# Kernel optimization log

Measured on AMD Instinct MI355X. Metric: run time of the kernel, lower is better.

The kernel has to match this reference:

```python
import jax, jax.numpy as jnp
import numpy as np

TOP_K = 2  # k experts per token


def setup_inputs() -> dict:
    key = jax.random.key(0)
    ks = jax.random.split(key, 6)
    B, L, D, E, F = 2, 2048, 1024, 8, 4096
    x = jax.random.normal(ks[0], (B, L, D), dtype=jnp.float32)
    Wg = jax.random.normal(ks[1], (D, E), dtype=jnp.float32) * (D ** -0.5)
    W1 = jax.random.normal(ks[2], (E, D, F), dtype=jnp.float32) * (D ** -0.5)
    b1 = jnp.zeros((E, F), dtype=jnp.float32)
    W2 = jax.random.normal(ks[3], (E, F, D), dtype=jnp.float32) * (F ** -0.5)
    b2 = jnp.zeros((E, D), dtype=jnp.float32)
    return {"x": x, "Wg": Wg, "W1": W1, "b1": b1, "W2": W2, "b2": b2}


def reference(x, Wg, W1, b1, W2, b2):
    b, l, d = x.shape
    E = Wg.shape[1]
    xt = x.reshape(b * l, d)                      # (N, D)
    N = xt.shape[0]
    # Router: sigmoid gate, top-k (gate weights are NOT renormalized in the source)
    S = jax.nn.sigmoid(xt @ Wg)                   # (N, E)
    G, I = jax.lax.top_k(S, TOP_K)                # (N, k) each
    # Dense equivalent of per-expert gather-MLP-scatter: run every expert
    # on every token, then combine with the sparse top-k routing weights.
    h = jax.nn.gelu(jnp.einsum('nd,edf->enf', xt, W1) + b1[:, None, :])  # (E, N, F)
    y = jnp.einsum('enf,efd->end', h, W2) + b2[:, None, :]               # (E, N, D)
    # combine[n, e] = sum of gate values for slots routed to expert e
    combine = jnp.zeros((N, E), dtype=x.dtype).at[jnp.arange(N)[:, None], I].add(G)
    out = jnp.einsum('ne,end->nd', combine, y)    # (N, D)
    return out.reshape(b, l, d)
```

## Files before the change

kernel.cpp:

```cpp
#include <hip/hip_runtime.h>
#include <math.h>

typedef __bf16 bf16_t;
typedef __attribute__((ext_vector_type(8))) __bf16 bf16x8;
typedef __attribute__((ext_vector_type(4))) __bf16 bf16x4;
typedef __attribute__((ext_vector_type(4))) float f32x4;

#define NTOK 4096
#define DDIM 1024
#define FDIM 4096
#define NEXP 8
#define CAP  4096
#define HROWS (2*NTOK + 128)
#define SPLITK2 4

#define GLOAD_LDS16(g, l) \
  __builtin_amdgcn_global_load_lds((__attribute__((address_space(1))) void*)(g), \
                                   (__attribute__((address_space(3))) void*)(l), 16, 0, 0)

__device__ __forceinline__ float fast_gelu(float v) {
  float u = 0.7978845608028654f * (v + 0.044715f * v * v * v);
  float uc = fminf(fmaxf(u, -10.f), 10.f);
  float t = __builtin_amdgcn_exp2f(2.885390081777927f * uc);
  float th = (t - 1.f) * __builtin_amdgcn_rcpf(t + 1.f);
  return 0.5f * v * (1.0f + th);
}

__global__ __launch_bounds__(256) void init_kernel(const float4* __restrict__ x4,
                                                   float4* __restrict__ out4,
                                                   bf16x4* __restrict__ xbf4,
                                                   int n4, int* __restrict__ cnts) {
  int i = blockIdx.x * 256 + threadIdx.x;
  if (i < n4) {
    out4[i] = make_float4(0.f, 0.f, 0.f, 0.f);
    float4 v = x4[i];
    bf16x4 o;
    o.x = (bf16_t)v.x; o.y = (bf16_t)v.y; o.z = (bf16_t)v.z; o.w = (bf16_t)v.w;
    xbf4[i] = o;
  }
  if (i < NEXP) cnts[i] = 0;
}

__global__ __launch_bounds__(256) void transpose_cvt(const float* __restrict__ in,
                                                     bf16_t* __restrict__ outp,
                                                     int R, int C) {
  __shared__ float tile[64][65];
  int e = blockIdx.z;
  const float* ip = in + (size_t)e * R * C;
  bf16_t* op = outp + (size_t)e * R * C;
  int c0 = blockIdx.x * 64, r0 = blockIdx.y * 64;
  int rr = threadIdx.x >> 4;
  int cc = (threadIdx.x & 15) * 4;
#pragma unroll
  for (int p = 0; p < 4; p++) {
    float4 v = *(const float4*)(ip + (size_t)(r0 + p * 16 + rr) * C + c0 + cc);
    tile[p * 16 + rr][cc + 0] = v.x;
    tile[p * 16 + rr][cc + 1] = v.y;
    tile[p * 16 + rr][cc + 2] = v.z;
    tile[p * 16 + rr][cc + 3] = v.w;
  }
  __syncthreads();
  int c = threadIdx.x >> 3;
  int r8 = (threadIdx.x & 7) * 8;
#pragma unroll
  for (int p = 0; p < 2; p++) {
    int cp = c + p * 32;
    bf16x8 o;
#pragma unroll
    for (int i = 0; i < 8; i++) o[i] = (bf16_t)tile[r8 + i][cp];
    *(bf16x8*)(op + (size_t)(c0 + cp) * R + r0 + r8) = o;
  }
}

__global__ __launch_bounds__(256) void router_kernel(const float* __restrict__ x,
                                                     const float* __restrict__ Wg,
                                                     int* __restrict__ tokL,
                                                     float* __restrict__ gateL,
                                                     int* __restrict__ cnts) {
  int wid = threadIdx.x >> 6, lane = threadIdx.x & 63;
  int n = blockIdx.x * 4 + wid;
  const float* xr = x + (size_t)n * DDIM;
  double acc[NEXP];
#pragma unroll
  for (int e = 0; e < NEXP; e++) acc[e] = 0.0;
  for (int i = 0; i < DDIM / 64; i++) {
    int d = i * 64 + lane;
    float xv = xr[d];
    const float* wr = Wg + (size_t)d * NEXP;
#pragma unroll
    for (int e = 0; e < NEXP; e++) acc[e] += (double)xv * (double)wr[e];
  }
#pragma unroll
  for (int e = 0; e < NEXP; e++) {
    double v = acc[e];
#pragma unroll
    for (int off = 32; off; off >>= 1) v += __shfl_xor(v, off);
    acc[e] = v;
  }
  if (lane == 0) {
    int i1 = -1, i2 = -1;
    double s1 = -1e300, s2 = -1e300;
#pragma unroll
    for (int e = 0; e < NEXP; e++) {
      double v = acc[e];
      if (v > s1) { s2 = s1; i2 = i1; s1 = v; i1 = e; }
      else if (v > s2) { s2 = v; i2 = e; }
    }
    float g1 = 1.0f / (1.0f + expf((float)(-s1)));
    float g2 = 1.0f / (1.0f + expf((float)(-s2)));
    int p1 = atomicAdd(&cnts[i1], 1);
    tokL[i1 * CAP + p1] = n; gateL[i1 * CAP + p1] = g1;
    int p2 = atomicAdd(&cnts[i2], 1);
    tokL[i2 * CAP + p2] = n; gateL[i2 * CAP + p2] = g2;
  }
}

__global__ void offs_kernel(const int* __restrict__ cnts, int* __restrict__ offs) {
  if (threadIdx.x == 0) {
    int s = 0;
    for (int e = 0; e < NEXP; e++) { offs[e] = s; s += cnts[e]; }
    offs[NEXP] = s;
  }
}

__global__ __launch_bounds__(256) void gemm1_kernel(
    const bf16_t* __restrict__ xbf, const bf16_t* __restrict__ wt1,
    const float* __restrict__ b1, const int* __restrict__ tokL,
    const int* __restrict__ cnts, const int* __restrict__ offs,
    bf16_t* __restrict__ H) {
  const int e = blockIdx.z;
  const int cnt = cnts[e];
  const int m0 = blockIdx.y * 128;
  if (m0 >= cnt) return;
  const int n0 = blockIdx.x * 128;
  const int t = threadIdx.x;

  __shared__ alignas(16) bf16_t As[128 * 32];
  __shared__ alignas(16) bf16_t Bs[128 * 32];

  const int sr = t >> 2;
  const int sc = (t & 3) * 8;
  const int r0 = m0 + sr, r1 = m0 + sr + 64;
  const int tok0 = (r0 < cnt) ? tokL[e * CAP + r0] : 0;
  const int tok1 = (r1 < cnt) ? tokL[e * CAP + r1] : 0;
  const bf16_t* gA0 = xbf + (size_t)tok0 * DDIM + sc;
  const bf16_t* gA1 = xbf + (size_t)tok1 * DDIM + sc;
  const bf16_t* wte = wt1 + (size_t)e * FDIM * DDIM;
  const bf16_t* gB0 = wte + (size_t)(n0 + sr) * DDIM + sc;
  const bf16_t* gB1 = wte + (size_t)(n0 + sr + 64) * DDIM + sc;
  bf16_t* lA0 = As + t * 8; bf16_t* lA1 = As + 2048 + t * 8;
  bf16_t* lB0 = Bs + t * 8; bf16_t* lB1 = Bs + 2048 + t * 8;

  const int lane = t & 63, w = t >> 6;
  const int wm = (w >> 1) * 64, wn = (w & 1) * 64;
  const int lid = lane & 15, quad = lane >> 4;

  f32x4 acc[4][4] = {};
  for (int kk = 0; kk < DDIM; kk += 32) {
    GLOAD_LDS16(gA0 + kk, lA0);
    GLOAD_LDS16(gA1 + kk, lA1);
    GLOAD_LDS16(gB0 + kk, lB0);
    GLOAD_LDS16(gB1 + kk, lB1);
    __syncthreads();
    bf16x8 af[4], bfm[4];
#pragma unroll
    for (int i = 0; i < 4; i++)
      af[i] = *(const bf16x8*)(As + (wm + i * 16 + lid) * 32 + quad * 8);
#pragma unroll
    for (int j = 0; j < 4; j++)
      bfm[j] = *(const bf16x8*)(Bs + (wn + j * 16 + lid) * 32 + quad * 8);
#pragma unroll
    for (int i = 0; i < 4; i++)
#pragma unroll
      for (int j = 0; j < 4; j++)
        acc[i][j] = __builtin_amdgcn_mfma_f32_16x16x32_bf16(af[i], bfm[j], acc[i][j], 0, 0, 0);
    __syncthreads();
  }

  const float* b1e = b1 + (size_t)e * FDIM;
  const int offe = offs[e];
#pragma unroll
  for (int i = 0; i < 4; i++) {
#pragma unroll
    for (int reg = 0; reg < 4; reg++) {
      int pos = m0 + wm + i * 16 + quad * 4 + reg;
      if (pos >= cnt) continue;
      size_t hrow = (size_t)(offe + pos);
#pragma unroll
      for (int j = 0; j < 4; j++) {
        int col = n0 + wn + j * 16 + lid;
        float v = acc[i][j][reg] + b1e[col];
        H[hrow * FDIM + col] = (bf16_t)fast_gelu(v);
      }
    }
  }
}

__global__ __launch_bounds__(256) void gemm2_kernel(
    const bf16_t* __restrict__ H, const bf16_t* __restrict__ wt2,
    const float* __restrict__ b2, const int* __restrict__ tokL,
    const float* __restrict__ gateL, const int* __restrict__ cnts,
    const int* __restrict__ offs, float* __restrict__ out) {
  const int e = blockIdx.z;
  const int cnt = cnts[e];
  const int by = blockIdx.y;
  const int m0 = (by / SPLITK2) * 128;
  const int split = by % SPLITK2;
  if (m0 >= cnt) return;
  const int n0 = blockIdx.x * 128;
  const int t = threadIdx.x;
  const int offe = offs[e];
  const int k0 = split * (FDIM / SPLITK2);

  __shared__ alignas(16) bf16_t As[128 * 32];
  __shared__ alignas(16) bf16_t Bs[128 * 32];

  const int sr = t >> 2;
  const int sc = (t & 3) * 8;
  const bf16_t* gA0 = H + (size_t)(offe + m0 + sr) * FDIM + sc + k0;
  const bf16_t* gA1 = H + (size_t)(offe + m0 + sr + 64) * FDIM + sc + k0;
  const bf16_t* wte = wt2 + (size_t)e * DDIM * FDIM;
  const bf16_t* gB0 = wte + (size_t)(n0 + sr) * FDIM + sc + k0;
  const bf16_t* gB1 = wte + (size_t)(n0 + sr + 64) * FDIM + sc + k0;
  bf16_t* lA0 = As + t * 8; bf16_t* lA1 = As + 2048 + t * 8;
  bf16_t* lB0 = Bs + t * 8; bf16_t* lB1 = Bs + 2048 + t * 8;

  const int lane = t & 63, w = t >> 6;
  const int wm = (w >> 1) * 64, wn = (w & 1) * 64;
  const int lid = lane & 15, quad = lane >> 4;

  f32x4 acc[4][4] = {};
  for (int kk = 0; kk < FDIM / SPLITK2; kk += 32) {
    GLOAD_LDS16(gA0 + kk, lA0);
    GLOAD_LDS16(gA1 + kk, lA1);
    GLOAD_LDS16(gB0 + kk, lB0);
    GLOAD_LDS16(gB1 + kk, lB1);
    __syncthreads();
    bf16x8 af[4], bfm[4];
#pragma unroll
    for (int i = 0; i < 4; i++)
      af[i] = *(const bf16x8*)(As + (wm + i * 16 + lid) * 32 + quad * 8);
#pragma unroll
    for (int j = 0; j < 4; j++)
      bfm[j] = *(const bf16x8*)(Bs + (wn + j * 16 + lid) * 32 + quad * 8);
#pragma unroll
    for (int i = 0; i < 4; i++)
#pragma unroll
      for (int j = 0; j < 4; j++)
        acc[i][j] = __builtin_amdgcn_mfma_f32_16x16x32_bf16(af[i], bfm[j], acc[i][j], 0, 0, 0);
    __syncthreads();
  }

  const float* b2e = b2 + (size_t)e * DDIM;
#pragma unroll
  for (int i = 0; i < 4; i++) {
#pragma unroll
    for (int reg = 0; reg < 4; reg++) {
      int pos = m0 + wm + i * 16 + quad * 4 + reg;
      if (pos >= cnt) continue;
      int tok = tokL[e * CAP + pos];
      float gate = gateL[e * CAP + pos];
#pragma unroll
      for (int j = 0; j < 4; j++) {
        int col = n0 + wn + j * 16 + lid;
        float v = acc[i][j][reg] + ((split == 0) ? b2e[col] : 0.f);
        atomicAdd(out + (size_t)tok * DDIM + col, gate * v);
      }
    }
  }
}

extern "C" void kernel_launch(void* const* d_in, const int* in_sizes, int n_in,
                              void* d_out, int out_size, void* d_ws, size_t ws_size,
                              hipStream_t stream) {
  const float* x  = (const float*)d_in[0];
  const float* Wg = (const float*)d_in[1];
  const float* W1 = (const float*)d_in[2];
  const float* b1 = (const float*)d_in[3];
  const float* W2 = (const float*)d_in[4];
  const float* b2 = (const float*)d_in[5];
  float* out = (float*)d_out;

  char* ws = (char*)d_ws;
  size_t off = 0;
  auto alloc = [&](size_t bytes) -> void* {
    void* p = (void*)(ws + off);
    off += (bytes + 255) & ~(size_t)255;
    return p;
  };
  bf16_t* xbf   = (bf16_t*)alloc((size_t)NTOK * DDIM * 2);
  bf16_t* wt1   = (bf16_t*)alloc((size_t)NEXP * FDIM * DDIM * 2);
  bf16_t* wt2   = (bf16_t*)alloc((size_t)NEXP * DDIM * FDIM * 2);
  bf16_t* H     = (bf16_t*)alloc((size_t)HROWS * FDIM * 2);
  int*    tokL  = (int*)alloc((size_t)NEXP * CAP * 4);
  float*  gateL = (float*)alloc((size_t)NEXP * CAP * 4);
  int*    cnts  = (int*)alloc(64);
  int*    offs  = (int*)alloc(64);
  if (off > ws_size) return;

  const int n4 = NTOK * DDIM / 4;
  init_kernel<<<(n4 + 255) / 256, 256, 0, stream>>>((const float4*)x, (float4*)out,
                                                    (bf16x4*)xbf, n4, cnts);
  transpose_cvt<<<dim3(FDIM / 64, DDIM / 64, NEXP), 256, 0, stream>>>(W1, wt1, DDIM, FDIM);
  transpose_cvt<<<dim3(DDIM / 64, FDIM / 64, NEXP), 256, 0, stream>>>(W2, wt2, FDIM, DDIM);
  router_kernel<<<NTOK / 4, 256, 0, stream>>>(x, Wg, tokL, gateL, cnts);
  offs_kernel<<<1, 64, 0, stream>>>(cnts, offs);
  gemm1_kernel<<<dim3(FDIM / 128, CAP / 128, NEXP), 256, 0, stream>>>(
      xbf, wt1, b1, tokL, cnts, offs, H);
  gemm2_kernel<<<dim3(DDIM / 128, (CAP / 128) * SPLITK2, NEXP), 256, 0, stream>>>(
      H, wt2, b2, tokL, gateL, cnts, offs, out);
}
```

Before: 746.1 us.

## Replace atomic scatter in gemm2 with per-pair buffers and a combine kernel

gemm2 now uses split-K of 2 instead of 4 and writes plain fp32 partial results into two buffers indexed by expert-sorted row, reusing the wt1 workspace, instead of atomically adding gated results into the output. A new combine kernel gathers each token's two routed rows, adds the bias, applies the gate weights and writes the output directly. This removes the output zeroing and the float atomics, at the cost of extra global traffic for the Y buffers and one more launch. Halving split-K also halves the number of gemm2 blocks.

```diff
diff --git a/kernel.cpp b/kernel.cpp
--- a/kernel.cpp
+++ b/kernel.cpp
@@ -12,7 +12,7 @@
 #define NEXP 8
 #define CAP  4096
 #define HROWS (2*NTOK + 128)
-#define SPLITK2 4
+#define NPAIR (2*NTOK)
 
 #define GLOAD_LDS16(g, l) \
   __builtin_amdgcn_global_load_lds((__attribute__((address_space(1))) void*)(g), \
@@ -27,12 +27,10 @@
 }
 
 __global__ __launch_bounds__(256) void init_kernel(const float4* __restrict__ x4,
-                                                   float4* __restrict__ out4,
                                                    bf16x4* __restrict__ xbf4,
                                                    int n4, int* __restrict__ cnts) {
   int i = blockIdx.x * 256 + threadIdx.x;
   if (i < n4) {
-    out4[i] = make_float4(0.f, 0.f, 0.f, 0.f);
     float4 v = x4[i];
     bf16x4 o;
     o.x = (bf16_t)v.x; o.y = (bf16_t)v.y; o.z = (bf16_t)v.z; o.w = (bf16_t)v.w;
@@ -75,8 +73,10 @@
 __global__ __launch_bounds__(256) void router_kernel(const float* __restrict__ x,
                                                      const float* __restrict__ Wg,
                                                      int* __restrict__ tokL,
-                                                     float* __restrict__ gateL,
-                                                     int* __restrict__ cnts) {
+                                                     int* __restrict__ cnts,
+                                                     int* __restrict__ pairE,
+                                                     int* __restrict__ pairS,
+                                                     float* __restrict__ pairG) {
   int wid = threadIdx.x >> 6, lane = threadIdx.x & 63;
   int n = blockIdx.x * 4 + wid;
   const float* xr = x + (size_t)n * DDIM;
@@ -109,9 +109,11 @@
     float g1 = 1.0f / (1.0f + expf((float)(-s1)));
     float g2 = 1.0f / (1.0f + expf((float)(-s2)));
     int p1 = atomicAdd(&cnts[i1], 1);
-    tokL[i1 * CAP + p1] = n; gateL[i1 * CAP + p1] = g1;
+    tokL[i1 * CAP + p1] = n;
     int p2 = atomicAdd(&cnts[i2], 1);
-    tokL[i2 * CAP + p2] = n; gateL[i2 * CAP + p2] = g2;
+    tokL[i2 * CAP + p2] = n;
+    pairE[2 * n] = i1; pairS[2 * n] = p1; pairG[2 * n] = g1;
+    pairE[2 * n + 1] = i2; pairS[2 * n + 1] = p2; pairG[2 * n + 1] = g2;
   }
 }
 
@@ -198,19 +200,18 @@
 
 __global__ __launch_bounds__(256) void gemm2_kernel(
     const bf16_t* __restrict__ H, const bf16_t* __restrict__ wt2,
-    const float* __restrict__ b2, const int* __restrict__ tokL,
-    const float* __restrict__ gateL, const int* __restrict__ cnts,
-    const int* __restrict__ offs, float* __restrict__ out) {
+    const int* __restrict__ cnts, const int* __restrict__ offs,
+    float* __restrict__ Y0, float* __restrict__ Y1) {
   const int e = blockIdx.z;
   const int cnt = cnts[e];
   const int by = blockIdx.y;
-  const int m0 = (by / SPLITK2) * 128;
-  const int split = by % SPLITK2;
+  const int m0 = (by >> 1) * 128;
+  const int split = by & 1;
   if (m0 >= cnt) return;
   const int n0 = blockIdx.x * 128;
   const int t = threadIdx.x;
   const int offe = offs[e];
-  const int k0 = split * (FDIM / SPLITK2);
+  const int k0 = split * (FDIM / 2);
 
   __shared__ alignas(16) bf16_t As[128 * 32];
   __shared__ alignas(16) bf16_t Bs[128 * 32];
@@ -230,7 +231,7 @@
   const int lid = lane & 15, quad = lane >> 4;
 
   f32x4 acc[4][4] = {};
-  for (int kk = 0; kk < FDIM / SPLITK2; kk += 32) {
+  for (int kk = 0; kk < FDIM / 2; kk += 32) {
     GLOAD_LDS16(gA0 + kk, lA0);
     GLOAD_LDS16(gA1 + kk, lA1);
     GLOAD_LDS16(gB0 + kk, lB0);
@@ -251,23 +252,48 @@
     __syncthreads();
   }
 
-  const float* b2e = b2 + (size_t)e * DDIM;
+  float* Ye = split ? Y1 : Y0;
 #pragma unroll
   for (int i = 0; i < 4; i++) {
 #pragma unroll
     for (int reg = 0; reg < 4; reg++) {
       int pos = m0 + wm + i * 16 + quad * 4 + reg;
       if (pos >= cnt) continue;
-      int tok = tokL[e * CAP + pos];
-      float gate = gateL[e * CAP + pos];
+      float* yrow = Ye + (size_t)(offe + pos) * DDIM;
 #pragma unroll
       for (int j = 0; j < 4; j++) {
         int col = n0 + wn + j * 16 + lid;
-        float v = acc[i][j][reg] + ((split == 0) ? b2e[col] : 0.f);
-        atomicAdd(out + (size_t)tok * DDIM + col, gate * v);
+        yrow[col] = acc[i][j][reg];
       }
     }
   }
+}
+
+__global__ __launch_bounds__(256) void combine_kernel(
+    const float* __restrict__ Y0, const float* __restrict__ Y1,
+    const float* __restrict__ b2, const int* __restrict__ pairE,
+    const int* __restrict__ pairS, const float* __restrict__ pairG,
+    const int* __restrict__ offs, float4* __restrict__ out4) {
+  const int n = blockIdx.x;
+  const int e1 = pairE[2 * n], e2 = pairE[2 * n + 1];
+  const int r1 = offs[e1] + pairS[2 * n];
+  const int r2 = offs[e2] + pairS[2 * n + 1];
+  const float g1 = pairG[2 * n], g2 = pairG[2 * n + 1];
+  const int t = threadIdx.x;
+  const float4* ya0 = (const float4*)(Y0 + (size_t)r1 * DDIM);
+  const float4* ya1 = (const float4*)(Y1 + (size_t)r1 * DDIM);
+  const float4* yb0 = (const float4*)(Y0 + (size_t)r2 * DDIM);
+  const float4* yb1 = (const float4*)(Y1 + (size_t)r2 * DDIM);
+  const float4* ba = (const float4*)(b2 + (size_t)e1 * DDIM);
+  const float4* bb = (const float4*)(b2 + (size_t)e2 * DDIM);
+  float4 a0 = ya0[t], a1 = ya1[t], c0 = yb0[t], c1 = yb1[t];
+  float4 pa = ba[t], pb = bb[t];
+  float4 o;
+  o.x = g1 * (a0.x + a1.x + pa.x) + g2 * (c0.x + c1.x + pb.x);
+  o.y = g1 * (a0.y + a1.y + pa.y) + g2 * (c0.y + c1.y + pb.y);
+  o.z = g1 * (a0.z + a1.z + pa.z) + g2 * (c0.z + c1.z + pb.z);
+  o.w = g1 * (a0.w + a1.w + pa.w) + g2 * (c0.w + c1.w + pb.w);
+  out4[(size_t)n * (DDIM / 4) + t] = o;
 }
 
 extern "C" void kernel_launch(void* const* d_in, const int* in_sizes, int n_in,
@@ -293,20 +319,28 @@
   bf16_t* wt2   = (bf16_t*)alloc((size_t)NEXP * DDIM * FDIM * 2);
   bf16_t* H     = (bf16_t*)alloc((size_t)HROWS * FDIM * 2);
   int*    tokL  = (int*)alloc((size_t)NEXP * CAP * 4);
-  float*  gateL = (float*)alloc((size_t)NEXP * CAP * 4);
+  int*    pairE = (int*)alloc((size_t)NPAIR * 4);
+  int*    pairS = (int*)alloc((size_t)NPAIR * 4);
+  float*  pairG = (float*)alloc((size_t)NPAIR * 4);
   int*    cnts  = (int*)alloc(64);
   int*    offs  = (int*)alloc(64);
   if (off > ws_size) return;
 
+  float* Y0 = (float*)wt1;
+  float* Y1 = Y0 + (size_t)NPAIR * DDIM / 2 * 2;
+  Y1 = Y0 + (size_t)8192 * DDIM;
+
   const int n4 = NTOK * DDIM / 4;
-  init_kernel<<<(n4 + 255) / 256, 256, 0, stream>>>((const float4*)x, (float4*)out,
-                                                    (bf16x4*)xbf, n4, cnts);
+  init_kernel<<<(n4 + 255) / 256, 256, 0, stream>>>((const float4*)x, (bf16x4*)xbf,
+                                                    n4, cnts);
   transpose_cvt<<<dim3(FDIM / 64, DDIM / 64, NEXP), 256, 0, stream>>>(W1, wt1, DDIM, FDIM);
   transpose_cvt<<<dim3(DDIM / 64, FDIM / 64, NEXP), 256, 0, stream>>>(W2, wt2, FDIM, DDIM);
-  router_kernel<<<NTOK / 4, 256, 0, stream>>>(x, Wg, tokL, gateL, cnts);
+  router_kernel<<<NTOK / 4, 256, 0, stream>>>(x, Wg, tokL, cnts, pairE, pairS, pairG);
   offs_kernel<<<1, 64, 0, stream>>>(cnts, offs);
   gemm1_kernel<<<dim3(FDIM / 128, CAP / 128, NEXP), 256, 0, stream>>>(
       xbf, wt1, b1, tokL, cnts, offs, H);
-  gemm2_kernel<<<dim3(DDIM / 128, (CAP / 128) * SPLITK2, NEXP), 256, 0, stream>>>(
-      H, wt2, b2, tokL, gateL, cnts, offs, out);
-}
+  gemm2_kernel<<<dim3(DDIM / 128, (CAP / 128) * 2, NEXP), 256, 0, stream>>>(
+      H, wt2, cnts, offs, Y0, Y1);
+  combine_kernel<<<NTOK, 256, 0, stream>>>(Y0, Y1, b2, pairE, pairS, pairG, offs,
+                                           (float4*)out);
+}
```

After: 703.5 us. 5.7% less time.
